# Optimization experiments

Measured on AMD Instinct MI355X. Metric: run time of the kernel, lower is better.

Reference implementation:

```python
import jax, jax.numpy as jnp
import numpy as np

MAX_OFFSET = 1.0  # kernel_size // 2


def _conv(x, w, groups=1):
    k = w.shape[-1]
    p = k // 2
    return jax.lax.conv_general_dilated(
        x, w, window_strides=(1, 1), padding=((p, p), (p, p)),
        dimension_numbers=('NCHW', 'OIHW', 'NCHW'), feature_group_count=groups)


def _reflect(coord, size):
    # torch grid_sample padding_mode='reflection', align_corners=False:
    # reflect over [-0.5, size-0.5], then clip to [0, size-1]
    span = float(size)
    xr = jnp.abs(coord + 0.5)
    extra = jnp.mod(xr, span)
    flips = jnp.floor(xr / span)
    out = jnp.where(jnp.mod(flips, 2.0) == 0.0, extra - 0.5, span - extra - 0.5)
    return jnp.clip(out, 0.0, size - 1)


def _grid_sample_bilinear_reflect(x, gx, gy):
    # x: (B,C,H,W); gx,gy: (B,H,W) normalized to [-1,1]
    b, c, h, w = x.shape
    # unnormalize (align_corners=False)
    ix = _reflect(((gx + 1.0) * w - 1.0) * 0.5, w)
    iy = _reflect(((gy + 1.0) * h - 1.0) * 0.5, h)
    ix0 = jnp.floor(ix); iy0 = jnp.floor(iy)
    wx1 = ix - ix0; wy1 = iy - iy0
    wx0 = 1.0 - wx1; wy0 = 1.0 - wy1
    ix0i = jnp.clip(ix0.astype(jnp.int32), 0, w - 1)
    iy0i = jnp.clip(iy0.astype(jnp.int32), 0, h - 1)
    ix1i = jnp.clip(ix0i + 1, 0, w - 1)
    iy1i = jnp.clip(iy0i + 1, 0, h - 1)
    bi = jnp.arange(b)[:, None, None]

    def g(iy_, ix_):
        return x[bi, :, iy_, ix_]  # (B,H,W,C)

    out = (g(iy0i, ix0i) * (wy0 * wx0)[..., None]
           + g(iy0i, ix1i) * (wy0 * wx1)[..., None]
           + g(iy1i, ix0i) * (wy1 * wx0)[..., None]
           + g(iy1i, ix1i) * (wy1 * wx1)[..., None])
    return jnp.transpose(out, (0, 3, 1, 2))  # (B,C,H,W)


def setup_inputs() -> dict:
    key = jax.random.key(0)
    k0, k1, k2 = jax.random.split(key, 3)
    b, c, h, w = 8, 32, 384, 384
    x = jax.random.normal(k0, (b, c, h, w), jnp.float32)
    offset_w = jax.random.normal(k1, (2, c, 3, 3), jnp.float32) * 0.1
    offset_b = jnp.zeros((2,), jnp.float32)
    dw_w = jax.random.normal(k2, (c, 1, 3, 3), jnp.float32) * 0.2
    return {"x": x, "offset_w": offset_w, "offset_b": offset_b, "dw_w": dw_w}


def reference(x, offset_w, offset_b, dw_w):
    b, c, h, w = x.shape
    offset = _conv(x, offset_w) + offset_b[None, :, None, None]  # (B,2,H,W)
    offset = jnp.tanh(offset) * MAX_OFFSET
    xx = jnp.arange(w, dtype=x.dtype)
    yy = jnp.arange(h, dtype=x.dtype)
    fx = xx[None, None, :] + offset[:, 0]  # (B,H,W)
    fy = yy[None, :, None] + offset[:, 1]
    gx = 2.0 * fx / max(w - 1, 1) - 1.0
    gy = 2.0 * fy / max(h - 1, 1) - 1.0
    x_def = _grid_sample_bilinear_reflect(x, gx, gy)
    out = _conv(x_def, dw_w, groups=c)
    return jax.nn.relu(out)
```

## Files before the change

kernel.cpp:

```cpp
#include <hip/hip_runtime.h>
#include <math.h>

#define B 8
#define C 32
#define H 384
#define W 384
#define HW (H*W)

typedef float f4 __attribute__((ext_vector_type(4)));
typedef float f2 __attribute__((ext_vector_type(2)));

__device__ __attribute__((aligned(16))) float ZERO_TILE[4];

__device__ __forceinline__ void gl_lds16(const float* gsrc, float* lds_dst) {
    __builtin_amdgcn_global_load_lds(
        (const __attribute__((address_space(1))) void*)gsrc,
        (__attribute__((address_space(3))) void*)lds_dst,
        16, 0, 0);
}

__device__ __forceinline__ float fast_tanh(float v) {
    float t = __expf(2.0f * v);
    return 1.0f - 2.0f / (t + 1.0f);
}

__device__ __forceinline__ float reflect_fast(float coord, float span) {
    float xr = fabsf(coord + 0.5f);
    float out = (xr < span) ? (xr - 0.5f) : (2.0f * span - xr - 0.5f);
    return fminf(fmaxf(out, 0.0f), span - 1.0f);
}

#define K1R 18
#define K1S 72
#define K1_SLOTS (K1R * 18)

__global__ __launch_bounds__(256) void offset_kernel(
        const float* __restrict__ x,
        const float* __restrict__ ow,
        const float* __restrict__ ob,
        float2* __restrict__ ws) {
    __shared__ float xs[2][2][K1R * K1S];

    const int tid = threadIdx.x;
    const int b_ = blockIdx.z;
    const int h0 = blockIdx.y * 16;
    const int w0 = blockIdx.x * 64;
    const float* xb = x + (size_t)b_ * C * HW;

    int  soff[2];
    bool sok[2];
    #pragma unroll
    for (int k = 0; k < 2; ++k) {
        int idx = tid + k * 256;
        int row = idx / 18, k4 = idx - row * 18;
        int grow = h0 - 1 + row;
        int gcol = w0 - 4 + k4 * 4;
        sok[k] = (idx < K1_SLOTS) && grow >= 0 && grow < H && gcol >= 0 && (gcol + 3) < W;
        soff[k] = max(grow, 0) * W + max(gcol, 0);
    }
    const int wbase0 = (tid >> 6) * 256;
    const int wbase1 = 1024 + (tid >> 6) * 256;

#define K1_STAGE(bufi, p) do {                                           \
        const float* xA_ = xb + (size_t)(2 * (p)) * HW;                  \
        const float* xB_ = xA_ + HW;                                     \
        gl_lds16(sok[0] ? (xA_ + soff[0]) : ZERO_TILE, &xs[bufi][0][wbase0]); \
        gl_lds16(sok[0] ? (xB_ + soff[0]) : ZERO_TILE, &xs[bufi][1][wbase0]); \
        if (tid < 68) {                                                  \
            gl_lds16(sok[1] ? (xA_ + soff[1]) : ZERO_TILE, &xs[bufi][0][wbase1]); \
            gl_lds16(sok[1] ? (xB_ + soff[1]) : ZERO_TILE, &xs[bufi][1][wbase1]); \
        }                                                                \
    } while (0)

    const int tx4 = (tid & 15) * 4;
    const int ty  = tid >> 4;

    float acc0[4], acc1[4];
    {
        float b0 = ob[0], b1 = ob[1];
        #pragma unroll
        for (int q = 0; q < 4; ++q) { acc0[q] = b0; acc1[q] = b1; }
    }

#define K1_CONV(bufp, wf0, wf1) do {                                     \
        _Pragma("unroll")                                                \
        for (int ky = 0; ky < 3; ++ky) {                                 \
            int base = (ty + ky) * K1S + tx4;                            \
            f4 A = *(const f4*)&(bufp)[base];                            \
            f4 Bv = *(const f4*)&(bufp)[base + 4];                       \
            float Cv = (bufp)[base + 8];                                 \
            float in[6] = {A.w, Bv.x, Bv.y, Bv.z, Bv.w, Cv};             \
            _Pragma("unroll")                                            \
            for (int q = 0; q < 4; ++q) {                                \
                acc0[q] = fmaf(in[q], wf0[ky*3+0], fmaf(in[q+1], wf0[ky*3+1], fmaf(in[q+2], wf0[ky*3+2], acc0[q]))); \
                acc1[q] = fmaf(in[q], wf1[ky*3+0], fmaf(in[q+1], wf1[ky*3+1], fmaf(in[q+2], wf1[ky*3+2], acc1[q]))); \
            }                                                            \
        }                                                                \
    } while (0)

    K1_STAGE(0, 0);
    __syncthreads();

    for (int p = 0; p < 16; ++p) {
        if (p + 1 < 16) K1_STAGE((p + 1) & 1, p + 1);

        const int ca = 2 * p, cb = 2 * p + 1;
        const float* wa0p = ow + ca * 9;
        const float* wa1p = ow + (C + ca) * 9;
        const float* wb0p = ow + cb * 9;
        const float* wb1p = ow + (C + cb) * 9;
        float wa0[9], wa1[9], wb0[9], wb1[9];
        #pragma unroll
        for (int k = 0; k < 9; ++k) {
            wa0[k] = wa0p[k]; wa1[k] = wa1p[k];
            wb0[k] = wb0p[k]; wb1[k] = wb1p[k];
        }

        K1_CONV(xs[p & 1][0], wa0, wa1);
        K1_CONV(xs[p & 1][1], wb0, wb1);

        __syncthreads();
    }

    const float sx = (float)W / (float)(W - 1);
    const float sy = (float)H / (float)(H - 1);
    const int hh = h0 + ty;
    float ixr[4], iyr[4];
    #pragma unroll
    for (int q = 0; q < 4; ++q) {
        float fx = (float)(w0 + tx4 + q) + fast_tanh(acc0[q]);
        float fy = (float)hh + fast_tanh(acc1[q]);
        ixr[q] = reflect_fast(fx * sx - 0.5f, (float)W);
        iyr[q] = reflect_fast(fy * sy - 0.5f, (float)H);
    }
    f4* p = (f4*)(ws + (size_t)b_ * HW + (size_t)hh * W + (w0 + tx4));
    f4 o0 = {ixr[0], iyr[0], ixr[1], iyr[1]};
    f4 o1 = {ixr[2], iyr[2], ixr[3], iyr[3]};
    p[0] = o0;
    p[1] = o1;
}

#define NC 8
#define XT_ROWS 22
#define XT_STRIDE 72
#define XT_N (XT_ROWS * XT_STRIDE)
#define XT_LOADS (XT_ROWS * 18)
#define XD_ROWS 18
#define XD_COLS 66
#define XD_STRIDE 68
#define META_N (XD_ROWS * XD_COLS)
#define K2_GX 6
#define K2_GY 24
#define K2_GZ (B * (C / NC))
#define K2_NWG (K2_GX * K2_GY * K2_GZ)
#define K2_CPX (K2_NWG / 8)

__global__ __launch_bounds__(256) void sample_dw_kernel(
        const float* __restrict__ x,
        const float2* __restrict__ ws,
        const float* __restrict__ dww,
        float* __restrict__ out) {
    __shared__ float xt[XT_N];
    __shared__ float xd[XD_ROWS * XD_STRIDE];
    __shared__ unsigned int m_addr[META_N];
    __shared__ float m_wx[META_N];
    __shared__ float m_wy[META_N];

    const int tid = threadIdx.x;
    const int id = blockIdx.x;
    const int nid = (id & 7) * K2_CPX + (id >> 3);
    const int bz = nid / (K2_GX * K2_GY);
    const int rem = nid - bz * (K2_GX * K2_GY);
    const int by = rem / K2_GX;
    const int bx = rem - by * K2_GX;

    const int b_ = bz >> 2;
    const int c0 = (bz & 3) * NC;
    const int h0 = by * 16;
    const int w0 = bx * 64;

    const float* xb = x + ((size_t)b_ * C + c0) * HW;
    const float2* wsb = ws + (size_t)b_ * HW;

    f4 pf[2];
    #pragma unroll
    for (int k = 0; k < 2; ++k) {
        int idx = tid + k * 256;
        f4 v = (f4)0.0f;
        if (idx < XT_LOADS) {
            int row = idx / 18, k4 = idx % 18;
            int grow = min(max(h0 - 3 + row, 0), H - 1);
            int gcol = min(max(w0 - 4 + k4 * 4, 0), W - 4);
            v = *(const f4*)(xb + grow * W + gcol);
        }
        pf[k] = v;
    }

    const int addr_base = (h0 - 3) * XT_STRIDE + (w0 - 4);
    #pragma unroll
    for (int k = 0; k < 5; ++k) {
        int i = tid + k * 256;
        if (i < META_N) {
            int r = i / XD_COLS, q = i - r * XD_COLS;
            int hp = h0 - 1 + r, wp = w0 - 1 + q;
            unsigned int addr = 0xFFFFFFFFu;
            float wx1 = 0.f, wy1 = 0.f;
            if (hp >= 0 && hp < H && wp >= 0 && wp < W) {
                float2 crd = wsb[hp * W + wp];
                float ix0f = floorf(crd.x), iy0f = floorf(crd.y);
                wx1 = crd.x - ix0f; wy1 = crd.y - iy0f;
                int ix0 = min(max((int)ix0f, 0), W - 1);
                int iy0 = min(max((int)iy0f, 0), H - 1);
                addr = (unsigned int)(iy0 * XT_STRIDE + ix0 - addr_base);
            }
            m_addr[i] = addr;
            m_wx[i] = wx1;
            m_wy[i] = wy1;
        }
    }
    __syncthreads();

    for (int cc = 0; cc < NC; ++cc) {
        #pragma unroll
        for (int k = 0; k < 2; ++k) {
            int idx = tid + k * 256;
            if (idx < XT_LOADS) {
                int row = idx / 18, k4 = idx % 18;
                *(f4*)&xt[row * XT_STRIDE + k4 * 4] = pf[k];
            }
        }
        __syncthreads();

        if (cc + 1 < NC) {
            const float* xc = xb + (size_t)(cc + 1) * HW;
            #pragma unroll
            for (int k = 0; k < 2; ++k) {
                int idx = tid + k * 256;
                f4 v = (f4)0.0f;
                if (idx < XT_LOADS) {
                    int row = idx / 18, k4 = idx % 18;
                    int grow = min(max(h0 - 3 + row, 0), H - 1);
                    int gcol = min(max(w0 - 4 + k4 * 4, 0), W - 4);
                    v = *(const f4*)(xc + grow * W + gcol);
                }
                pf[k] = v;
            }
        }

        #pragma unroll
        for (int k = 0; k < 5; ++k) {
            int i = tid + k * 256;
            if (i < META_N) {
                int r = i / XD_COLS, q = i - r * XD_COLS;
                unsigned int addr = m_addr[i];
                float v = 0.0f;
                if (addr != 0xFFFFFFFFu) {
                    float wx1 = m_wx[i], wy1 = m_wy[i];
                    float wx0 = 1.0f - wx1, wy0 = 1.0f - wy1;
                    float v00 = xt[addr];
                    float v01 = xt[addr + 1];
                    float v10 = xt[addr + XT_STRIDE];
                    float v11 = xt[addr + XT_STRIDE + 1];
                    v = (v00 * wx0 + v01 * wx1) * wy0 + (v10 * wx0 + v11 * wx1) * wy1;
                }
                xd[r * XD_STRIDE + q] = v;
            }
        }

        float wk[9];
        const float* wc = dww + (size_t)(c0 + cc) * 9;
        #pragma unroll
        for (int i = 0; i < 9; ++i) wk[i] = wc[i];

        __syncthreads();

        const int tx2 = (tid & 31) * 2;
        const int ty0 = (tid >> 5) * 2;
        float a[2][2] = {{0.f, 0.f}, {0.f, 0.f}};
        #pragma unroll
        for (int r = 0; r < 4; ++r) {
            const float* rowp = xd + (ty0 + r) * XD_STRIDE + tx2;
            f2 p0 = *(const f2*)rowp;
            f2 p1 = *(const f2*)(rowp + 2);
            #pragma unroll
            for (int ky = 0; ky < 3; ++ky) {
                int j = r - ky;
                if (j < 0 || j > 1) continue;
                a[j][0] = fmaf(p0.x, wk[ky*3+0], fmaf(p0.y, wk[ky*3+1], fmaf(p1.x, wk[ky*3+2], a[j][0])));
                a[j][1] = fmaf(p0.y, wk[ky*3+0], fmaf(p1.x, wk[ky*3+1], fmaf(p1.y, wk[ky*3+2], a[j][1])));
            }
        }
        float* outc = out + ((size_t)b_ * C + c0 + cc) * HW;
        #pragma unroll
        for (int j = 0; j < 2; ++j) {
            f2 res;
            res.x = fmaxf(a[j][0], 0.0f);
            res.y = fmaxf(a[j][1], 0.0f);
            __builtin_nontemporal_store(res,
                (f2*)&outc[(size_t)(h0 + ty0 + j) * W + (w0 + tx2)]);
        }
        __syncthreads();
    }
}

extern "C" void kernel_launch(void* const* d_in, const int* in_sizes, int n_in,
                              void* d_out, int out_size, void* d_ws, size_t ws_size,
                              hipStream_t stream) {
    const float* x   = (const float*)d_in[0];
    const float* ow  = (const float*)d_in[1];
    const float* ob  = (const float*)d_in[2];
    const float* dww = (const float*)d_in[3];
    float* out = (float*)d_out;
    float2* ws = (float2*)d_ws;

    dim3 g1(W / 64, H / 16, B);
    offset_kernel<<<g1, 256, 0, stream>>>(x, ow, ob, ws);

    sample_dw_kernel<<<dim3(K2_NWG), 256, 0, stream>>>(x, ws, dww, out);
}
```

Before: 110.1 us.

## Pack sample coordinates as 16-bit fixed-point relative offsets and swizzle offset grid

The offset kernel now stores each pixel's reflected sampling coordinate as two 16-bit fixed-point offsets relative to the pixel position, packed into one 32-bit word instead of a float2. This halves the intermediate workspace traffic between the two kernels. The offset kernel also switches to a 1D grid with an XCD-aware block remapping, matching the sampling kernel. The quantization step of 1/16384 adds a small rounding error to the bilinear weights, and the packing assumes the relative offset stays within about ±2 pixels.

```diff
diff --git a/kernel.cpp b/kernel.cpp
--- a/kernel.cpp
+++ b/kernel.cpp
@@ -9,6 +9,7 @@
 
 typedef float f4 __attribute__((ext_vector_type(4)));
 typedef float f2 __attribute__((ext_vector_type(2)));
+typedef unsigned int u4 __attribute__((ext_vector_type(4)));
 
 __device__ __attribute__((aligned(16))) float ZERO_TILE[4];
 
@@ -30,21 +31,30 @@
     return fminf(fmaxf(out, 0.0f), span - 1.0f);
 }
 
+#define INV_SCALE 6.103515625e-5f
+
 #define K1R 18
 #define K1S 72
 #define K1_SLOTS (K1R * 18)
+#define K1_NWG 1152
+#define K1_CPX (K1_NWG / 8)
 
 __global__ __launch_bounds__(256) void offset_kernel(
         const float* __restrict__ x,
         const float* __restrict__ ow,
         const float* __restrict__ ob,
-        float2* __restrict__ ws) {
+        unsigned int* __restrict__ ws) {
     __shared__ float xs[2][2][K1R * K1S];
 
     const int tid = threadIdx.x;
-    const int b_ = blockIdx.z;
-    const int h0 = blockIdx.y * 16;
-    const int w0 = blockIdx.x * 64;
+    const int id = blockIdx.x;
+    const int nid = (id & 7) * K1_CPX + (id >> 3);
+    const int b_ = nid / 144;
+    const int rem = nid - b_ * 144;
+    const int by = rem / 6;
+    const int bx = rem - by * 6;
+    const int h0 = by * 16;
+    const int w0 = bx * 64;
     const float* xb = x + (size_t)b_ * C * HW;
 
     int  soff[2];
@@ -125,19 +135,19 @@
     const float sx = (float)W / (float)(W - 1);
     const float sy = (float)H / (float)(H - 1);
     const int hh = h0 + ty;
-    float ixr[4], iyr[4];
+    u4 pk;
     #pragma unroll
     for (int q = 0; q < 4; ++q) {
-        float fx = (float)(w0 + tx4 + q) + fast_tanh(acc0[q]);
+        float wwp = (float)(w0 + tx4 + q);
+        float fx = wwp + fast_tanh(acc0[q]);
         float fy = (float)hh + fast_tanh(acc1[q]);
-        ixr[q] = reflect_fast(fx * sx - 0.5f, (float)W);
-        iyr[q] = reflect_fast(fy * sy - 0.5f, (float)H);
-    }
-    f4* p = (f4*)(ws + (size_t)b_ * HW + (size_t)hh * W + (w0 + tx4));
-    f4 o0 = {ixr[0], iyr[0], ixr[1], iyr[1]};
-    f4 o1 = {ixr[2], iyr[2], ixr[3], iyr[3]};
-    p[0] = o0;
-    p[1] = o1;
+        float ixr = reflect_fast(fx * sx - 0.5f, (float)W);
+        float iyr = reflect_fast(fy * sy - 0.5f, (float)H);
+        unsigned int ux = (unsigned int)((ixr - wwp + 2.0f) * 16384.0f + 0.5f);
+        unsigned int uy = (unsigned int)((iyr - (float)hh + 2.0f) * 16384.0f + 0.5f);
+        pk[q] = ux | (uy << 16);
+    }
+    *(u4*)&ws[(size_t)b_ * HW + (size_t)hh * W + (w0 + tx4)] = pk;
 }
 
 #define NC 8
@@ -157,7 +167,7 @@
 
 __global__ __launch_bounds__(256) void sample_dw_kernel(
         const float* __restrict__ x,
-        const float2* __restrict__ ws,
+        const unsigned int* __restrict__ ws,
         const float* __restrict__ dww,
         float* __restrict__ out) {
     __shared__ float xt[XT_N];
@@ -180,7 +190,7 @@
     const int w0 = bx * 64;
 
     const float* xb = x + ((size_t)b_ * C + c0) * HW;
-    const float2* wsb = ws + (size_t)b_ * HW;
+    const unsigned int* wsb = ws + (size_t)b_ * HW;
 
     f4 pf[2];
     #pragma unroll
@@ -206,9 +216,11 @@
             unsigned int addr = 0xFFFFFFFFu;
             float wx1 = 0.f, wy1 = 0.f;
             if (hp >= 0 && hp < H && wp >= 0 && wp < W) {
-                float2 crd = wsb[hp * W + wp];
-                float ix0f = floorf(crd.x), iy0f = floorf(crd.y);
-                wx1 = crd.x - ix0f; wy1 = crd.y - iy0f;
+                unsigned int cu = wsb[hp * W + wp];
+                float ix = (float)wp + (float)(cu & 0xFFFFu) * INV_SCALE - 2.0f;
+                float iy = (float)hp + (float)(cu >> 16)     * INV_SCALE - 2.0f;
+                float ix0f = floorf(ix), iy0f = floorf(iy);
+                wx1 = ix - ix0f; wy1 = iy - iy0f;
                 int ix0 = min(max((int)ix0f, 0), W - 1);
                 int iy0 = min(max((int)iy0f, 0), H - 1);
                 addr = (unsigned int)(iy0 * XT_STRIDE + ix0 - addr_base);
@@ -311,10 +323,8 @@
     const float* ob  = (const float*)d_in[2];
     const float* dww = (const float*)d_in[3];
     float* out = (float*)d_out;
-    float2* ws = (float2*)d_ws;
-
-    dim3 g1(W / 64, H / 16, B);
-    offset_kernel<<<g1, 256, 0, stream>>>(x, ow, ob, ws);
-
+    unsigned int* ws = (unsigned int*)d_ws;
+
+    offset_kernel<<<dim3(K1_NWG), 256, 0, stream>>>(x, ow, ob, ws);
     sample_dw_kernel<<<dim3(K2_NWG), 256, 0, stream>>>(x, ws, dww, out);
 }
```

Measured after the change: 95.23 us. -13.5%, faster.
